# Optimization experiments

Measured on AMD Instinct MI355X. Metric: run time of the kernel, lower is better.

## Reference

```python
import jax, jax.numpy as jnp
import numpy as np

N, E = 100000, 800000
INPUTS, HIDDEN = 64, 64
EPS = 1e-5


def setup_inputs() -> dict:
    key = jax.random.key(0)
    ks = jax.random.split(key, 16)
    d_in = INPUTS + HIDDEN  # 128, input dim of both MLPs

    def lin_init(k, fan_in, fan_out):
        # torch Linear default init: U(-1/sqrt(fan_in), 1/sqrt(fan_in))
        kw, kb = jax.random.split(k)
        bound = 1.0 / np.sqrt(fan_in)
        W = jax.random.uniform(kw, (fan_in, fan_out), jnp.float32, -bound, bound)
        b = jax.random.uniform(kb, (fan_out,), jnp.float32, -bound, bound)
        return W, b

    W1a, b1a = lin_init(ks[0], d_in, HIDDEN)
    W2a, b2a = lin_init(ks[1], HIDDEN, HIDDEN)
    W1b, b1b = lin_init(ks[2], d_in, HIDDEN)
    W2b, b2b = lin_init(ks[3], HIDDEN, HIDDEN)

    return {
        "x": jax.random.normal(ks[4], (N, INPUTS), jnp.float32),
        "edge_index": jax.random.randint(ks[5], (2, E), 0, N, jnp.int64),
        "edge_attr": jax.random.normal(ks[6], (E, HIDDEN), jnp.float32),
        "u": jax.random.normal(ks[7], (1, 8), jnp.float32),
        "batch": jnp.zeros((N,), jnp.int64),
        "W1a": W1a, "b1a": b1a,
        "g1": jnp.ones((HIDDEN,), jnp.float32), "be1": jnp.zeros((HIDDEN,), jnp.float32),
        "W2a": W2a, "b2a": b2a,
        "W1b": W1b, "b1b": b1b,
        "g2": jnp.ones((HIDDEN,), jnp.float32), "be2": jnp.zeros((HIDDEN,), jnp.float32),
        "W2b": W2b, "b2b": b2b,
    }


def _mlp(h, W1, b1, g, be, W2, b2):
    # Lin -> BatchNorm1d (training-mode batch stats, biased var) -> ReLU -> Lin
    h = h @ W1 + b1
    mu = jnp.mean(h, axis=0)
    var = jnp.var(h, axis=0)
    h = (h - mu) * jax.lax.rsqrt(var + EPS) * g + be
    h = jax.nn.relu(h)
    return h @ W2 + b2


def reference(x, edge_index, edge_attr, u, batch,
              W1a, b1a, g1, be1, W2a, b2a,
              W1b, b1b, g2, be2, W2b, b2b):
    row, col = edge_index[0], edge_index[1]
    n = x.shape[0]
    # gather source-node features, concat with edge features: [E, inputs+hidden]
    out = jnp.concatenate([x[row], edge_attr], axis=1)
    out = _mlp(out, W1a, b1a, g1, be1, W2a, b2a)
    # scatter_mean over destination nodes
    summed = jax.ops.segment_sum(out, col, num_segments=n)
    cnt = jax.ops.segment_sum(jnp.ones((out.shape[0],), out.dtype), col, num_segments=n)
    mean = summed / jnp.maximum(cnt, 1.0)[:, None]
    out = jnp.concatenate([x, mean], axis=1)
    return _mlp(out, W1b, b1b, g2, be2, W2b, b2b)
```

## Files before the change

kernel.cpp:

```cpp
#include <hip/hip_runtime.h>
#include <hip/hip_bf16.h>
#include <cstddef>
#include <cstdint>

#define N_NODES 100000
#define N_EDGES 800000
#define EPS 1e-5f

typedef __attribute__((ext_vector_type(8))) short bf16x8;
typedef __attribute__((ext_vector_type(4))) float f32x4;
typedef __attribute__((ext_vector_type(8))) unsigned short u16x8;

#define MFMA16(a, b, c) __builtin_amdgcn_mfma_f32_16x16x32_bf16(a, b, c, 0, 0, 0)

__device__ __forceinline__ unsigned short f2bf(float f) {
  return __builtin_bit_cast(unsigned short, __float2bfloat16(f));
}
__device__ __forceinline__ float bf2f(unsigned short u) {
  return __bfloat162float(__builtin_bit_cast(__hip_bfloat16, u));
}

__device__ __forceinline__ bf16x8 cvt8(const float* __restrict__ p) {
  float4 u = *(const float4*)p;
  float4 v = *(const float4*)(p + 4);
  bf16x8 r;
  r[0] = (short)f2bf(u.x); r[1] = (short)f2bf(u.y);
  r[2] = (short)f2bf(u.z); r[3] = (short)f2bf(u.w);
  r[4] = (short)f2bf(v.x); r[5] = (short)f2bf(v.y);
  r[6] = (short)f2bf(v.z); r[7] = (short)f2bf(v.w);
  return r;
}

__device__ __forceinline__ bf16x8 cvt8s(const float* __restrict__ p, float s) {
  float4 u = *(const float4*)p;
  float4 v = *(const float4*)(p + 4);
  bf16x8 r;
  r[0] = (short)f2bf(u.x * s); r[1] = (short)f2bf(u.y * s);
  r[2] = (short)f2bf(u.z * s); r[3] = (short)f2bf(u.w * s);
  r[4] = (short)f2bf(v.x * s); r[5] = (short)f2bf(v.y * s);
  r[6] = (short)f2bf(v.z * s); r[7] = (short)f2bf(v.w * s);
  return r;
}

__global__ void prep_w(const float* __restrict__ W1a, const float* __restrict__ W2a,
                       const float* __restrict__ W1b, const float* __restrict__ W2b,
                       unsigned short* __restrict__ wt) {
  int i = blockIdx.x * 256 + threadIdx.x;
  if (i >= 24576) return;
  if (i < 8192) {
    int n = i >> 7, k = i & 127;
    wt[i] = f2bf(W1a[k * 64 + n]);
  } else if (i < 12288) {
    int j = i - 8192; int n = j >> 6, k = j & 63;
    wt[i] = f2bf(W2a[k * 64 + n]);
  } else if (i < 20480) {
    int j = i - 12288; int n = j >> 7, k = j & 127;
    wt[i] = f2bf(W1b[k * 64 + n]);
  } else {
    int j = i - 20480; int n = j >> 6, k = j & 63;
    wt[i] = f2bf(W2b[k * 64 + n]);
  }
}

__global__ void count_edges(const int* __restrict__ ei_col, float* __restrict__ cnt) {
  int e = blockIdx.x * 256 + threadIdx.x;
  if (e < N_EDGES) atomicAdd(&cnt[ei_col[e]], 1.f);
}

__global__ void bn_finalize(const float* __restrict__ st, const float* __restrict__ g,
                            const float* __restrict__ be, float* __restrict__ scsh,
                            float inv_count) {
  int j = threadIdx.x;
  float s = 0.f, q = 0.f;
  for (int k = 0; k < 64; k++) { s += st[k * 128 + j]; q += st[k * 128 + 64 + j]; }
  float mu = s * inv_count;
  float var = q * inv_count - mu * mu;
  float sc = g[j] * rsqrtf(var + EPS);
  scsh[j] = sc;
  scsh[64 + j] = be[j] - mu * sc;
}

__global__ __launch_bounds__(256, 4)
void edge_mlp1_mfma(const float* __restrict__ x, const int* __restrict__ ei_row,
                    const float* __restrict__ ea, const unsigned short* __restrict__ Wt,
                    const float* __restrict__ b1,
                    unsigned short* __restrict__ h1, float* __restrict__ stats) {
  __shared__ unsigned short Wl[64 * 136];
  __shared__ int rows[128];
  int tid = threadIdx.x;
  int base = blockIdx.x * 128;
  if (tid < 128) rows[tid] = ei_row[base + tid];
#pragma unroll
  for (int i = 0; i < 4; i++) {
    int g = i * 256 + tid;
    int n = g >> 4, k0 = (g & 15) * 8;
    *(u16x8*)&Wl[n * 136 + k0] = *(const u16x8*)&Wt[n * 128 + k0];
  }
  __syncthreads();

  int l = tid & 63, w = tid >> 6;
  int m16 = l & 15, g4 = l >> 4;
  int er0 = w * 32 + m16, er1 = er0 + 16;

  const float* xp0 = &x[(size_t)rows[er0] * 64 + g4 * 8];
  const float* xp1 = &x[(size_t)rows[er1] * 64 + g4 * 8];
  const float* ep0 = &ea[(size_t)(base + er0) * 64 + g4 * 8];
  const float* ep1 = &ea[(size_t)(base + er1) * 64 + g4 * 8];

  bf16x8 a[2][4];
  a[0][0] = cvt8(xp0);      a[0][1] = cvt8(xp0 + 32);
  a[1][0] = cvt8(xp1);      a[1][1] = cvt8(xp1 + 32);
  a[0][2] = cvt8(ep0);      a[0][3] = cvt8(ep0 + 32);
  a[1][2] = cvt8(ep1);      a[1][3] = cvt8(ep1 + 32);

  f32x4 acc[2][4];
#pragma unroll
  for (int nt = 0; nt < 4; nt++) {
    float bv = b1[nt * 16 + m16];
#pragma unroll
    for (int mt = 0; mt < 2; mt++) acc[mt][nt] = (f32x4){bv, bv, bv, bv};
  }
#pragma unroll
  for (int kit = 0; kit < 4; kit++) {
    bf16x8 b[4];
#pragma unroll
    for (int nt = 0; nt < 4; nt++)
      b[nt] = *(const bf16x8*)&Wl[(nt * 16 + m16) * 136 + kit * 32 + g4 * 8];
#pragma unroll
    for (int mt = 0; mt < 2; mt++)
#pragma unroll
      for (int nt = 0; nt < 4; nt++)
        acc[mt][nt] = MFMA16(a[mt][kit], b[nt], acc[mt][nt]);
  }

  float ps[4] = {0, 0, 0, 0}, pq[4] = {0, 0, 0, 0};
#pragma unroll
  for (int mt = 0; mt < 2; mt++) {
    int erow = base + w * 32 + mt * 16 + g4 * 4;
#pragma unroll
    for (int nt = 0; nt < 4; nt++) {
      int ch = nt * 16 + m16;
#pragma unroll
      for (int r = 0; r < 4; r++) {
        float v = acc[mt][nt][r];
        h1[(size_t)(erow + r) * 64 + ch] = f2bf(v);
        ps[nt] += v; pq[nt] += v * v;
      }
    }
  }
#pragma unroll
  for (int nt = 0; nt < 4; nt++) {
    ps[nt] += __shfl_xor(ps[nt], 16); ps[nt] += __shfl_xor(ps[nt], 32);
    pq[nt] += __shfl_xor(pq[nt], 16); pq[nt] += __shfl_xor(pq[nt], 32);
  }
  float ssel = (g4 == 0) ? ps[0] : (g4 == 1) ? ps[1] : (g4 == 2) ? ps[2] : ps[3];
  float qsel = (g4 == 0) ? pq[0] : (g4 == 1) ? pq[1] : (g4 == 2) ? pq[2] : pq[3];
  int slot = blockIdx.x & 63;
  atomicAdd(&stats[slot * 128 + l], ssel);
  atomicAdd(&stats[slot * 128 + 64 + l], qsel);
}

__global__ __launch_bounds__(256, 4)
void node_mlp1_mfma(const float* __restrict__ x, const float* __restrict__ ns,
                    const float* __restrict__ cnt, const unsigned short* __restrict__ Wt,
                    const float* __restrict__ b1,
                    unsigned short* __restrict__ h2, float* __restrict__ stats) {
  __shared__ unsigned short Wl[64 * 136];
  int tid = threadIdx.x;
  int base = blockIdx.x * 128;
#pragma unroll
  for (int i = 0; i < 4; i++) {
    int g = i * 256 + tid;
    int n = g >> 4, k0 = (g & 15) * 8;
    *(u16x8*)&Wl[n * 136 + k0] = *(const u16x8*)&Wt[n * 128 + k0];
  }
  __syncthreads();

  int l = tid & 63, w = tid >> 6;
  int m16 = l & 15, g4 = l >> 4;
  int r0 = base + w * 32 + m16, r1 = r0 + 16;
  int c0 = (r0 < N_NODES) ? r0 : 0;
  int c1 = (r1 < N_NODES) ? r1 : 0;
  float inv0 = 1.f / fmaxf(cnt[c0], 1.f);
  float inv1 = 1.f / fmaxf(cnt[c1], 1.f);

  const float* xp0 = &x[(size_t)c0 * 64 + g4 * 8];
  const float* xp1 = &x[(size_t)c1 * 64 + g4 * 8];
  const float* np0 = &ns[(size_t)c0 * 64 + g4 * 8];
  const float* np1 = &ns[(size_t)c1 * 64 + g4 * 8];

  bf16x8 a[2][4];
  a[0][0] = cvt8(xp0);           a[0][1] = cvt8(xp0 + 32);
  a[1][0] = cvt8(xp1);           a[1][1] = cvt8(xp1 + 32);
  a[0][2] = cvt8s(np0, inv0);    a[0][3] = cvt8s(np0 + 32, inv0);
  a[1][2] = cvt8s(np1, inv1);    a[1][3] = cvt8s(np1 + 32, inv1);

  f32x4 acc[2][4];
#pragma unroll
  for (int nt = 0; nt < 4; nt++) {
    float bv = b1[nt * 16 + m16];
#pragma unroll
    for (int mt = 0; mt < 2; mt++) acc[mt][nt] = (f32x4){bv, bv, bv, bv};
  }
#pragma unroll
  for (int kit = 0; kit < 4; kit++) {
    bf16x8 b[4];
#pragma unroll
    for (int nt = 0; nt < 4; nt++)
      b[nt] = *(const bf16x8*)&Wl[(nt * 16 + m16) * 136 + kit * 32 + g4 * 8];
#pragma unroll
    for (int mt = 0; mt < 2; mt++)
#pragma unroll
      for (int nt = 0; nt < 4; nt++)
        acc[mt][nt] = MFMA16(a[mt][kit], b[nt], acc[mt][nt]);
  }

  float ps[4] = {0, 0, 0, 0}, pq[4] = {0, 0, 0, 0};
#pragma unroll
  for (int mt = 0; mt < 2; mt++) {
    int nrow = base + w * 32 + mt * 16 + g4 * 4;
#pragma unroll
    for (int nt = 0; nt < 4; nt++) {
      int ch = nt * 16 + m16;
#pragma unroll
      for (int r = 0; r < 4; r++) {
        float v = acc[mt][nt][r];
        if (nrow + r < N_NODES) {
          h2[(size_t)(nrow + r) * 64 + ch] = f2bf(v);
          ps[nt] += v; pq[nt] += v * v;
        }
      }
    }
  }
#pragma unroll
  for (int nt = 0; nt < 4; nt++) {
    ps[nt] += __shfl_xor(ps[nt], 16); ps[nt] += __shfl_xor(ps[nt], 32);
    pq[nt] += __shfl_xor(pq[nt], 16); pq[nt] += __shfl_xor(pq[nt], 32);
  }
  float ssel = (g4 == 0) ? ps[0] : (g4 == 1) ? ps[1] : (g4 == 2) ? ps[2] : ps[3];
  float qsel = (g4 == 0) ? pq[0] : (g4 == 1) ? pq[1] : (g4 == 2) ? pq[2] : pq[3];
  int slot = blockIdx.x & 63;
  atomicAdd(&stats[slot * 128 + l], ssel);
  atomicAdd(&stats[slot * 128 + 64 + l], qsel);
}

__global__ __launch_bounds__(256, 4)
void edge_mlp2_mfma(const unsigned short* __restrict__ h1, const int* __restrict__ ei_col,
                    const unsigned short* __restrict__ Wt2, const float* __restrict__ b2,
                    const float* __restrict__ scsh, float* __restrict__ nodesum) {
  __shared__ unsigned short Wl[64 * 72];
  __shared__ int cols[128];
  int tid = threadIdx.x;
  int base = blockIdx.x * 128;
  if (tid < 128) cols[tid] = ei_col[base + tid];
#pragma unroll
  for (int i = 0; i < 2; i++) {
    int g = i * 256 + tid;
    int n = g >> 3, k0 = (g & 7) * 8;
    *(u16x8*)&Wl[n * 72 + k0] = *(const u16x8*)&Wt2[n * 64 + k0];
  }
  __syncthreads();

  int l = tid & 63, w = tid >> 6;
  int m16 = l & 15, g4 = l >> 4;
  int er0 = w * 32 + m16, er1 = er0 + 16;

  float sc[2][8], sh[2][8];
#pragma unroll
  for (int kit = 0; kit < 2; kit++) {
    int k = kit * 32 + g4 * 8;
    float4 s0 = *(const float4*)&scsh[k];
    float4 s1 = *(const float4*)&scsh[k + 4];
    float4 t0 = *(const float4*)&scsh[64 + k];
    float4 t1 = *(const float4*)&scsh[64 + k + 4];
    sc[kit][0] = s0.x; sc[kit][1] = s0.y; sc[kit][2] = s0.z; sc[kit][3] = s0.w;
    sc[kit][4] = s1.x; sc[kit][5] = s1.y; sc[kit][6] = s1.z; sc[kit][7] = s1.w;
    sh[kit][0] = t0.x; sh[kit][1] = t0.y; sh[kit][2] = t0.z; sh[kit][3] = t0.w;
    sh[kit][4] = t1.x; sh[kit][5] = t1.y; sh[kit][6] = t1.z; sh[kit][7] = t1.w;
  }

  bf16x8 a[2][2];
#pragma unroll
  for (int mt = 0; mt < 2; mt++) {
    const unsigned short* hp = &h1[(size_t)(base + (mt ? er1 : er0)) * 64 + g4 * 8];
#pragma unroll
    for (int kit = 0; kit < 2; kit++) {
      u16x8 hv = *(const u16x8*)(hp + kit * 32);
      bf16x8 o;
#pragma unroll
      for (int j = 0; j < 8; j++) {
        float v = fmaxf(fmaf(bf2f(hv[j]), sc[kit][j], sh[kit][j]), 0.f);
        o[j] = (short)f2bf(v);
      }
      a[mt][kit] = o;
    }
  }

  f32x4 acc[2][4];
#pragma unroll
  for (int nt = 0; nt < 4; nt++) {
    float bv = b2[nt * 16 + m16];
#pragma unroll
    for (int mt = 0; mt < 2; mt++) acc[mt][nt] = (f32x4){bv, bv, bv, bv};
  }
#pragma unroll
  for (int kit = 0; kit < 2; kit++) {
    bf16x8 b[4];
#pragma unroll
    for (int nt = 0; nt < 4; nt++)
      b[nt] = *(const bf16x8*)&Wl[(nt * 16 + m16) * 72 + kit * 32 + g4 * 8];
#pragma unroll
    for (int mt = 0; mt < 2; mt++)
#pragma unroll
      for (int nt = 0; nt < 4; nt++)
        acc[mt][nt] = MFMA16(a[mt][kit], b[nt], acc[mt][nt]);
  }
#pragma unroll
  for (int mt = 0; mt < 2; mt++) {
#pragma unroll
    for (int r = 0; r < 4; r++) {
      int el = w * 32 + mt * 16 + g4 * 4 + r;
      int node = cols[el];
#pragma unroll
      for (int nt = 0; nt < 4; nt++) {
        int ch = nt * 16 + m16;
        atomicAdd(&nodesum[(size_t)node * 64 + ch], acc[mt][nt][r]);
      }
    }
  }
}

__global__ __launch_bounds__(256, 4)
void node_mlp2_mfma(const unsigned short* __restrict__ h2, const unsigned short* __restrict__ Wt2,
                    const float* __restrict__ b2, const float* __restrict__ scsh,
                    float* __restrict__ out) {
  __shared__ unsigned short Wl[64 * 72];
  int tid = threadIdx.x;
  int base = blockIdx.x * 128;
#pragma unroll
  for (int i = 0; i < 2; i++) {
    int g = i * 256 + tid;
    int n = g >> 3, k0 = (g & 7) * 8;
    *(u16x8*)&Wl[n * 72 + k0] = *(const u16x8*)&Wt2[n * 64 + k0];
  }
  __syncthreads();

  int l = tid & 63, w = tid >> 6;
  int m16 = l & 15, g4 = l >> 4;
  int r0 = base + w * 32 + m16, r1 = r0 + 16;
  int c0 = (r0 < N_NODES) ? r0 : 0;
  int c1 = (r1 < N_NODES) ? r1 : 0;

  float sc[2][8], sh[2][8];
#pragma unroll
  for (int kit = 0; kit < 2; kit++) {
    int k = kit * 32 + g4 * 8;
    float4 s0 = *(const float4*)&scsh[k];
    float4 s1 = *(const float4*)&scsh[k + 4];
    float4 t0 = *(const float4*)&scsh[64 + k];
    float4 t1 = *(const float4*)&scsh[64 + k + 4];
    sc[kit][0] = s0.x; sc[kit][1] = s0.y; sc[kit][2] = s0.z; sc[kit][3] = s0.w;
    sc[kit][4] = s1.x; sc[kit][5] = s1.y; sc[kit][6] = s1.z; sc[kit][7] = s1.w;
    sh[kit][0] = t0.x; sh[kit][1] = t0.y; sh[kit][2] = t0.z; sh[kit][3] = t0.w;
    sh[kit][4] = t1.x; sh[kit][5] = t1.y; sh[kit][6] = t1.z; sh[kit][7] = t1.w;
  }

  bf16x8 a[2][2];
#pragma unroll
  for (int mt = 0; mt < 2; mt++) {
    const unsigned short* hp = &h2[(size_t)(mt ? c1 : c0) * 64 + g4 * 8];
#pragma unroll
    for (int kit = 0; kit < 2; kit++) {
      u16x8 hv = *(const u16x8*)(hp + kit * 32);
      bf16x8 o;
#pragma unroll
      for (int j = 0; j < 8; j++) {
        float v = fmaxf(fmaf(bf2f(hv[j]), sc[kit][j], sh[kit][j]), 0.f);
        o[j] = (short)f2bf(v);
      }
      a[mt][kit] = o;
    }
  }

  f32x4 acc[2][4];
#pragma unroll
  for (int nt = 0; nt < 4; nt++) {
    float bv = b2[nt * 16 + m16];
#pragma unroll
    for (int mt = 0; mt < 2; mt++) acc[mt][nt] = (f32x4){bv, bv, bv, bv};
  }
#pragma unroll
  for (int kit = 0; kit < 2; kit++) {
    bf16x8 b[4];
#pragma unroll
    for (int nt = 0; nt < 4; nt++)
      b[nt] = *(const bf16x8*)&Wl[(nt * 16 + m16) * 72 + kit * 32 + g4 * 8];
#pragma unroll
    for (int mt = 0; mt < 2; mt++)
#pragma unroll
      for (int nt = 0; nt < 4; nt++)
        acc[mt][nt] = MFMA16(a[mt][kit], b[nt], acc[mt][nt]);
  }
#pragma unroll
  for (int mt = 0; mt < 2; mt++) {
    int nrow = base + w * 32 + mt * 16 + g4 * 4;
#pragma unroll
    for (int nt = 0; nt < 4; nt++) {
      int ch = nt * 16 + m16;
#pragma unroll
      for (int r = 0; r < 4; r++) {
        if (nrow + r < N_NODES) out[(size_t)(nrow + r) * 64 + ch] = acc[mt][nt][r];
      }
    }
  }
}

extern "C" void kernel_launch(void* const* d_in, const int* in_sizes, int n_in,
                              void* d_out, int out_size, void* d_ws, size_t ws_size,
                              hipStream_t stream) {
  const float* x   = (const float*)d_in[0];
  const int*   ei  = (const int*)d_in[1];
  const float* ea  = (const float*)d_in[2];
  const float* W1a = (const float*)d_in[5];
  const float* b1a = (const float*)d_in[6];
  const float* g1  = (const float*)d_in[7];
  const float* be1 = (const float*)d_in[8];
  const float* W2a = (const float*)d_in[9];
  const float* b2a = (const float*)d_in[10];
  const float* W1b = (const float*)d_in[11];
  const float* b1b = (const float*)d_in[12];
  const float* g2  = (const float*)d_in[13];
  const float* be2 = (const float*)d_in[14];
  const float* W2b = (const float*)d_in[15];
  const float* b2b = (const float*)d_in[16];
  float* out = (float*)d_out;

  char* p = (char*)d_ws;
  unsigned short* h1 = (unsigned short*)p;      p += (size_t)N_EDGES * 64 * 2;
  float* nodesum = (float*)p;                   p += (size_t)N_NODES * 64 * 4;
  float* cnt = (float*)p;                       p += (size_t)N_NODES * 4;
  float* stats1 = (float*)p;                    p += 8192 * 4;
  float* stats2 = (float*)p;                    p += 8192 * 4;
  float* scsh1 = (float*)p;                     p += 128 * 4;
  float* scsh2 = (float*)p;                     p += 128 * 4;
  unsigned short* h2 = (unsigned short*)p;      p += (size_t)N_NODES * 64 * 2;
  unsigned short* wt = (unsigned short*)p;
  unsigned short* wt1a = wt;
  unsigned short* wt2a = wt + 8192;
  unsigned short* wt1b = wt + 12288;
  unsigned short* wt2b = wt + 20480;

  size_t zbytes = (size_t)N_NODES * 64 * 4 + (size_t)N_NODES * 4 + 2 * 8192 * 4;
  (void)hipMemsetAsync(nodesum, 0, zbytes, stream);

  prep_w<<<96, 256, 0, stream>>>(W1a, W2a, W1b, W2b, wt);
  edge_mlp1_mfma<<<6250, 256, 0, stream>>>(x, ei, ea, wt1a, b1a, h1, stats1);
  bn_finalize<<<1, 64, 0, stream>>>(stats1, g1, be1, scsh1, 1.0f / (float)N_EDGES);
  count_edges<<<3125, 256, 0, stream>>>(ei + N_EDGES, cnt);
  edge_mlp2_mfma<<<6250, 256, 0, stream>>>(h1, ei + N_EDGES, wt2a, b2a, scsh1, nodesum);
  node_mlp1_mfma<<<782, 256, 0, stream>>>(x, nodesum, cnt, wt1b, b1b, h2, stats2);
  bn_finalize<<<1, 64, 0, stream>>>(stats2, g2, be2, scsh2, 1.0f / (float)N_NODES);
  node_mlp2_mfma<<<782, 256, 0, stream>>>(h2, wt2b, b2b, scsh2, out);
}
```

Before: 612.7 us.

## Sort edges by destination and apply second edge linear after mean aggregation

```diff
diff --git a/kernel.cpp b/kernel.cpp
--- a/kernel.cpp
+++ b/kernel.cpp
@@ -28,17 +28,6 @@
   r[2] = (short)f2bf(u.z); r[3] = (short)f2bf(u.w);
   r[4] = (short)f2bf(v.x); r[5] = (short)f2bf(v.y);
   r[6] = (short)f2bf(v.z); r[7] = (short)f2bf(v.w);
-  return r;
-}
-
-__device__ __forceinline__ bf16x8 cvt8s(const float* __restrict__ p, float s) {
-  float4 u = *(const float4*)p;
-  float4 v = *(const float4*)(p + 4);
-  bf16x8 r;
-  r[0] = (short)f2bf(u.x * s); r[1] = (short)f2bf(u.y * s);
-  r[2] = (short)f2bf(u.z * s); r[3] = (short)f2bf(u.w * s);
-  r[4] = (short)f2bf(v.x * s); r[5] = (short)f2bf(v.y * s);
-  r[6] = (short)f2bf(v.z * s); r[7] = (short)f2bf(v.w * s);
   return r;
 }
 
@@ -62,9 +51,42 @@
   }
 }
 
-__global__ void count_edges(const int* __restrict__ ei_col, float* __restrict__ cnt) {
+__global__ void count_edges_i(const int* __restrict__ ei_col, int* __restrict__ cnti) {
   int e = blockIdx.x * 256 + threadIdx.x;
-  if (e < N_EDGES) atomicAdd(&cnt[ei_col[e]], 1.f);
+  if (e < N_EDGES) atomicAdd(&cnti[ei_col[e]], 1);
+}
+
+#define SCAN_T 1024
+__global__ void scan_offsets(const int* __restrict__ cnti, int* __restrict__ off,
+                             int* __restrict__ cursor) {
+  __shared__ int part[SCAN_T];
+  int t = threadIdx.x;
+  const int chunk = (N_NODES + SCAN_T - 1) / SCAN_T;
+  int lo = t * chunk;
+  int hi = lo + chunk; if (hi > N_NODES) hi = N_NODES;
+  int s = 0;
+  for (int i = lo; i < hi; i++) s += cnti[i];
+  part[t] = s;
+  __syncthreads();
+  if (t == 0) {
+    int run = 0;
+    for (int i = 0; i < SCAN_T; i++) { int v = part[i]; part[i] = run; run += v; }
+  }
+  __syncthreads();
+  int run = part[t];
+  for (int i = lo; i < hi; i++) {
+    off[i] = run; cursor[i] = run;
+    run += cnti[i];
+  }
+}
+
+__global__ void rank_edges(const int* __restrict__ ei_col, int* __restrict__ cursor,
+                           int* __restrict__ rank) {
+  int e = blockIdx.x * 256 + threadIdx.x;
+  if (e < N_EDGES) {
+    int c = ei_col[e];
+    rank[e] = atomicAdd(&cursor[c], 1);
+  }
 }
 
 __global__ void bn_finalize(const float* __restrict__ st, const float* __restrict__ g,
@@ -82,14 +104,19 @@
 
 __global__ __launch_bounds__(256, 4)
 void edge_mlp1_mfma(const float* __restrict__ x, const int* __restrict__ ei_row,
-                    const float* __restrict__ ea, const unsigned short* __restrict__ Wt,
+                    const float* __restrict__ ea, const int* __restrict__ rank,
+                    const unsigned short* __restrict__ Wt,
                     const float* __restrict__ b1,
                     unsigned short* __restrict__ h1, float* __restrict__ stats) {
   __shared__ unsigned short Wl[64 * 136];
   __shared__ int rows[128];
+  __shared__ int rankl[128];
   int tid = threadIdx.x;
   int base = blockIdx.x * 128;
-  if (tid < 128) rows[tid] = ei_row[base + tid];
+  if (tid < 128) {
+    rows[tid] = ei_row[base + tid];
+    rankl[tid] = rank[base + tid];
+  }
 #pragma unroll
   for (int i = 0; i < 4; i++) {
     int g = i * 256 + tid;
@@ -136,14 +163,13 @@
   float ps[4] = {0, 0, 0, 0}, pq[4] = {0, 0, 0, 0};
 #pragma unroll
   for (int mt = 0; mt < 2; mt++) {
-    int erow = base + w * 32 + mt * 16 + g4 * 4;
-#pragma unroll
-    for (int nt = 0; nt < 4; nt++) {
-      int ch = nt * 16 + m16;
-#pragma unroll
-      for (int r = 0; r < 4; r++) {
+#pragma unroll
+    for (int r = 0; r < 4; r++) {
+      int prow = rankl[w * 32 + mt * 16 + g4 * 4 + r];
+#pragma unroll
+      for (int nt = 0; nt < 4; nt++) {
         float v = acc[mt][nt][r];
-        h1[(size_t)(erow + r) * 64 + ch] = f2bf(v);
+        h1[(size_t)prow * 64 + nt * 16 + m16] = f2bf(v);
         ps[nt] += v; pq[nt] += v * v;
       }
     }
@@ -160,9 +186,96 @@
   atomicAdd(&stats[slot * 128 + 64 + l], qsel);
 }
 
+__global__ __launch_bounds__(256)
+void gather_g(const unsigned short* __restrict__ h1, const int* __restrict__ off,
+              const int* __restrict__ cnti, const float* __restrict__ scsh,
+              unsigned short* __restrict__ g) {
+  int w = threadIdx.x >> 6, l = threadIdx.x & 63;
+  int n = blockIdx.x * 4 + w;
+  if (n >= N_NODES) return;
+  float sc = scsh[l], sh = scsh[64 + l];
+  int o = off[n], d = cnti[n];
+  float s = 0.f;
+  int i = 0;
+  for (; i + 2 <= d; i += 2) {
+    float v0 = bf2f(h1[(size_t)(o + i) * 64 + l]);
+    float v1 = bf2f(h1[(size_t)(o + i + 1) * 64 + l]);
+    s += fmaxf(fmaf(v0, sc, sh), 0.f);
+    s += fmaxf(fmaf(v1, sc, sh), 0.f);
+  }
+  if (i < d) {
+    float v0 = bf2f(h1[(size_t)(o + i) * 64 + l]);
+    s += fmaxf(fmaf(v0, sc, sh), 0.f);
+  }
+  float inv = (d > 0) ? (1.f / (float)d) : 1.f;
+  g[(size_t)n * 64 + l] = f2bf(s * inv);
+}
+
 __global__ __launch_bounds__(256, 4)
-void node_mlp1_mfma(const float* __restrict__ x, const float* __restrict__ ns,
-                    const float* __restrict__ cnt, const unsigned short* __restrict__ Wt,
+void node_agg_mfma(const unsigned short* __restrict__ g, const int* __restrict__ cnti,
+                   const unsigned short* __restrict__ Wt2, const float* __restrict__ b2,
+                   unsigned short* __restrict__ m) {
+  __shared__ unsigned short Wl[64 * 72];
+  int tid = threadIdx.x;
+  int base = blockIdx.x * 128;
+#pragma unroll
+  for (int i = 0; i < 2; i++) {
+    int gg = i * 256 + tid;
+    int n = gg >> 3, k0 = (gg & 7) * 8;
+    *(u16x8*)&Wl[n * 72 + k0] = *(const u16x8*)&Wt2[n * 64 + k0];
+  }
+  __syncthreads();
+
+  int l = tid & 63, w = tid >> 6;
+  int m16 = l & 15, g4 = l >> 4;
+  int r0 = base + w * 32 + m16, r1 = r0 + 16;
+  int c0 = (r0 < N_NODES) ? r0 : 0;
+  int c1 = (r1 < N_NODES) ? r1 : 0;
+
+  bf16x8 a[2][2];
+  a[0][0] = *(const bf16x8*)&g[(size_t)c0 * 64 + g4 * 8];
+  a[0][1] = *(const bf16x8*)&g[(size_t)c0 * 64 + 32 + g4 * 8];
+  a[1][0] = *(const bf16x8*)&g[(size_t)c1 * 64 + g4 * 8];
+  a[1][1] = *(const bf16x8*)&g[(size_t)c1 * 64 + 32 + g4 * 8];
+
+  f32x4 acc[2][4];
+#pragma unroll
+  for (int nt = 0; nt < 4; nt++) {
+    float bv = b2[nt * 16 + m16];
+#pragma unroll
+    for (int mt = 0; mt < 2; mt++) acc[mt][nt] = (f32x4){bv, bv, bv, bv};
+  }
+#pragma unroll
+  for (int kit = 0; kit < 2; kit++) {
+    bf16x8 b[4];
+#pragma unroll
+    for (int nt = 0; nt < 4; nt++)
+      b[nt] = *(const bf16x8*)&Wl[(nt * 16 + m16) * 72 + kit * 32 + g4 * 8];
+#pragma unroll
+    for (int mt = 0; mt < 2; mt++)
+#pragma unroll
+      for (int nt = 0; nt < 4; nt++)
+        acc[mt][nt] = MFMA16(a[mt][kit], b[nt], acc[mt][nt]);
+  }
+#pragma unroll
+  for (int mt = 0; mt < 2; mt++) {
+#pragma unroll
+    for (int r = 0; r < 4; r++) {
+      int row = base + w * 32 + mt * 16 + g4 * 4 + r;
+      if (row < N_NODES) {
+        bool nz = cnti[row] > 0;
+#pragma unroll
+        for (int nt = 0; nt < 4; nt++) {
+          m[(size_t)row * 64 + nt * 16 + m16] = nz ? f2bf(acc[mt][nt][r]) : (unsigned short)0;
+        }
+      }
+    }
+  }
+}
+
+__global__ __launch_bounds__(256, 4)
+void node_mlp1_mfma(const float* __restrict__ x, const unsigned short* __restrict__ m,
+                    const unsigned short* __restrict__ Wt,
                     const float* __restrict__ b1,
                     unsigned short* __restrict__ h2, float* __restrict__ stats) {
   __shared__ unsigned short Wl[64 * 136];
@@ -181,19 +294,17 @@
   int r0 = base + w * 32 + m16, r1 = r0 + 16;
   int c0 = (r0 < N_NODES) ? r0 : 0;
   int c1 = (r1 < N_NODES) ? r1 : 0;
-  float inv0 = 1.f / fmaxf(cnt[c0], 1.f);
-  float inv1 = 1.f / fmaxf(cnt[c1], 1.f);
 
   const float* xp0 = &x[(size_t)c0 * 64 + g4 * 8];
   const float* xp1 = &x[(size_t)c1 * 64 + g4 * 8];
-  const float* np0 = &ns[(size_t)c0 * 64 + g4 * 8];
-  const float* np1 = &ns[(size_t)c1 * 64 + g4 * 8];
 
   bf16x8 a[2][4];
-  a[0][0] = cvt8(xp0);           a[0][1] = cvt8(xp0 + 32);
-  a[1][0] = cvt8(xp1);           a[1][1] = cvt8(xp1 + 32);
-  a[0][2] = cvt8s(np0, inv0);    a[0][3] = cvt8s(np0 + 32, inv0);
-  a[1][2] = cvt8s(np1, inv1);    a[1][3] = cvt8s(np1 + 32, inv1);
+  a[0][0] = cvt8(xp0);      a[0][1] = cvt8(xp0 + 32);
+  a[1][0] = cvt8(xp1);      a[1][1] = cvt8(xp1 + 32);
+  a[0][2] = *(const bf16x8*)&m[(size_t)c0 * 64 + g4 * 8];
+  a[0][3] = *(const bf16x8*)&m[(size_t)c0 * 64 + 32 + g4 * 8];
+  a[1][2] = *(const bf16x8*)&m[(size_t)c1 * 64 + g4 * 8];
+  a[1][3] = *(const bf16x8*)&m[(size_t)c1 * 64 + 32 + g4 * 8];
 
   f32x4 acc[2][4];
 #pragma unroll
@@ -242,92 +353,6 @@
   int slot = blockIdx.x & 63;
   atomicAdd(&stats[slot * 128 + l], ssel);
   atomicAdd(&stats[slot * 128 + 64 + l], qsel);
-}
-
-__global__ __launch_bounds__(256, 4)
-void edge_mlp2_mfma(const unsigned short* __restrict__ h1, const int* __restrict__ ei_col,
-                    const unsigned short* __restrict__ Wt2, const float* __restrict__ b2,
-                    const float* __restrict__ scsh, float* __restrict__ nodesum) {
-  __shared__ unsigned short Wl[64 * 72];
-  __shared__ int cols[128];
-  int tid = threadIdx.x;
-  int base = blockIdx.x * 128;
-  if (tid < 128) cols[tid] = ei_col[base + tid];
-#pragma unroll
-  for (int i = 0; i < 2; i++) {
-    int g = i * 256 + tid;
-    int n = g >> 3, k0 = (g & 7) * 8;
-    *(u16x8*)&Wl[n * 72 + k0] = *(const u16x8*)&Wt2[n * 64 + k0];
-  }
-  __syncthreads();
-
-  int l = tid & 63, w = tid >> 6;
-  int m16 = l & 15, g4 = l >> 4;
-  int er0 = w * 32 + m16, er1 = er0 + 16;
-
-  float sc[2][8], sh[2][8];
-#pragma unroll
-  for (int kit = 0; kit < 2; kit++) {
-    int k = kit * 32 + g4 * 8;
-    float4 s0 = *(const float4*)&scsh[k];
-    float4 s1 = *(const float4*)&scsh[k + 4];
-    float4 t0 = *(const float4*)&scsh[64 + k];
-    float4 t1 = *(const float4*)&scsh[64 + k + 4];
-    sc[kit][0] = s0.x; sc[kit][1] = s0.y; sc[kit][2] = s0.z; sc[kit][3] = s0.w;
-    sc[kit][4] = s1.x; sc[kit][5] = s1.y; sc[kit][6] = s1.z; sc[kit][7] = s1.w;
-    sh[kit][0] = t0.x; sh[kit][1] = t0.y; sh[kit][2] = t0.z; sh[kit][3] = t0.w;
-    sh[kit][4] = t1.x; sh[kit][5] = t1.y; sh[kit][6] = t1.z; sh[kit][7] = t1.w;
-  }
-
-  bf16x8 a[2][2];
-#pragma unroll
-  for (int mt = 0; mt < 2; mt++) {
-    const unsigned short* hp = &h1[(size_t)(base + (mt ? er1 : er0)) * 64 + g4 * 8];
-#pragma unroll
-    for (int kit = 0; kit < 2; kit++) {
-      u16x8 hv = *(const u16x8*)(hp + kit * 32);
-      bf16x8 o;
-#pragma unroll
-      for (int j = 0; j < 8; j++) {
-        float v = fmaxf(fmaf(bf2f(hv[j]), sc[kit][j], sh[kit][j]), 0.f);
-        o[j] = (short)f2bf(v);
-      }
-      a[mt][kit] = o;
-    }
-  }
-
-  f32x4 acc[2][4];
-#pragma unroll
-  for (int nt = 0; nt < 4; nt++) {
-    float bv = b2[nt * 16 + m16];
-#pragma unroll
-    for (int mt = 0; mt < 2; mt++) acc[mt][nt] = (f32x4){bv, bv, bv, bv};
-  }
-#pragma unroll
-  for (int kit = 0; kit < 2; kit++) {
-    bf16x8 b[4];
-#pragma unroll
-    for (int nt = 0; nt < 4; nt++)
-      b[nt] = *(const bf16x8*)&Wl[(nt * 16 + m16) * 72 + kit * 32 + g4 * 8];
-#pragma unroll
-    for (int mt = 0; mt < 2; mt++)
-#pragma unroll
-      for (int nt = 0; nt < 4; nt++)
-        acc[mt][nt] = MFMA16(a[mt][kit], b[nt], acc[mt][nt]);
-  }
-#pragma unroll
-  for (int mt = 0; mt < 2; mt++) {
-#pragma unroll
-    for (int r = 0; r < 4; r++) {
-      int el = w * 32 + mt * 16 + g4 * 4 + r;
-      int node = cols[el];
-#pragma unroll
-      for (int nt = 0; nt < 4; nt++) {
-        int ch = nt * 16 + m16;
-        atomicAdd(&nodesum[(size_t)node * 64 + ch], acc[mt][nt][r]);
-      }
-    }
-  }
 }
 
 __global__ __launch_bounds__(256, 4)
@@ -436,29 +461,36 @@
   float* out = (float*)d_out;
 
   char* p = (char*)d_ws;
-  unsigned short* h1 = (unsigned short*)p;      p += (size_t)N_EDGES * 64 * 2;
-  float* nodesum = (float*)p;                   p += (size_t)N_NODES * 64 * 4;
-  float* cnt = (float*)p;                       p += (size_t)N_NODES * 4;
-  float* stats1 = (float*)p;                    p += 8192 * 4;
-  float* stats2 = (float*)p;                    p += 8192 * 4;
-  float* scsh1 = (float*)p;                     p += 128 * 4;
-  float* scsh2 = (float*)p;                     p += 128 * 4;
-  unsigned short* h2 = (unsigned short*)p;      p += (size_t)N_NODES * 64 * 2;
+  unsigned short* h1 = (unsigned short*)p;  p += (size_t)N_EDGES * 64 * 2;
+  unsigned short* gb = (unsigned short*)p;  p += (size_t)N_NODES * 64 * 2;
+  unsigned short* mb = (unsigned short*)p;  p += (size_t)N_NODES * 64 * 2;
+  int* cnti = (int*)p;                      p += (size_t)N_NODES * 4;
+  float* stats1 = (float*)p;                p += 8192 * 4;
+  float* stats2 = (float*)p;                p += 8192 * 4;
+  int* off = (int*)p;                       p += (size_t)N_NODES * 4;
+  int* cursor = (int*)p;                    p += (size_t)N_NODES * 4;
+  int* rank = (int*)p;                      p += (size_t)N_EDGES * 4;
+  float* scsh1 = (float*)p;                 p += 128 * 4;
+  float* scsh2 = (float*)p;                 p += 128 * 4;
+  unsigned short* h2 = (unsigned short*)p;  p += (size_t)N_NODES * 64 * 2;
   unsigned short* wt = (unsigned short*)p;
   unsigned short* wt1a = wt;
   unsigned short* wt2a = wt + 8192;
   unsigned short* wt1b = wt + 12288;
   unsigned short* wt2b = wt + 20480;
 
-  size_t zbytes = (size_t)N_NODES * 64 * 4 + (size_t)N_NODES * 4 + 2 * 8192 * 4;
-  (void)hipMemsetAsync(nodesum, 0, zbytes, stream);
+  size_t zbytes = (size_t)N_NODES * 4 + 2 * 8192 * 4;
+  (void)hipMemsetAsync(cnti, 0, zbytes, stream);
 
   prep_w<<<96, 256, 0, stream>>>(W1a, W2a, W1b, W2b, wt);
-  edge_mlp1_mfma<<<6250, 256, 0, stream>>>(x, ei, ea, wt1a, b1a, h1, stats1);
+  count_edges_i<<<3125, 256, 0, stream>>>(ei + N_EDGES, cnti);
+  scan_offsets<<<1, SCAN_T, 0, stream>>>(cnti, off, cursor);
+  rank_edges<<<3125, 256, 0, stream>>>(ei + N_EDGES, cursor, rank);
+  edge_mlp1_mfma<<<6250, 256, 0, stream>>>(x, ei, ea, rank, wt1a, b1a, h1, stats1);
   bn_finalize<<<1, 64, 0, stream>>>(stats1, g1, be1, scsh1, 1.0f / (float)N_EDGES);
-  count_edges<<<3125, 256, 0, stream>>>(ei + N_EDGES, cnt);
-  edge_mlp2_mfma<<<6250, 256, 0, stream>>>(h1, ei + N_EDGES, wt2a, b2a, scsh1, nodesum);
-  node_mlp1_mfma<<<782, 256, 0, stream>>>(x, nodesum, cnt, wt1b, b1b, h2, stats2);
+  gather_g<<<25000, 256, 0, stream>>>(h1, off, cnti, scsh1, gb);
+  node_agg_mfma<<<782, 256, 0, stream>>>(gb, cnti, wt2a, b2a, mb);
+  node_mlp1_mfma<<<782, 256, 0, stream>>>(x, mb, wt1b, b1b, h2, stats2);
   bn_finalize<<<1, 64, 0, stream>>>(stats2, g2, be2, scsh2, 1.0f / (float)N_NODES);
   node_mlp2_mfma<<<782, 256, 0, stream>>>(h2, wt2b, b2b, scsh2, out);
 }
```

After: 755.3 us. +23.3%, slower.
